# Kernel tuning notes

Measured on AMD Instinct MI355X. Metric: run time of the kernel, lower is better.

Reference implementation:

```python
import jax, jax.numpy as jnp
import numpy as np

B_, L, DM = 2, 1024, 1024
D_STATE, D_CONV, EXPAND = 16, 4, 2
DI = EXPAND * DM          # 2048 inner dim
DTR = DM // 16            # 64 dt rank


def setup_inputs() -> dict:
    key = jax.random.key(0)
    ks = jax.random.split(key, 16)
    g = lambda k, shp, s: jax.random.normal(k, shp, jnp.float32) * s
    inp = {
        "x": g(ks[0], (B_, L, DM), 1.0),
        "ln_g": jnp.ones((DM,), jnp.float32),
        "ln_b": jnp.zeros((DM,), jnp.float32),
        "in_proj_w": g(ks[1], (2 * DI, DM), (2.0 / (DM + 2 * DI)) ** 0.5),
        "conv_w": g(ks[2], (DI, 1, D_CONV), (2.0 / D_CONV) ** 0.5),
        "conv_b": jnp.zeros((DI,), jnp.float32),
        "dtin_w": g(ks[3], (DTR, DI), (2.0 / (DI + DTR)) ** 0.5),
        "dtin_b": jnp.zeros((DTR,), jnp.float32),
        "dt_w": g(ks[4], (DI, DTR), DTR ** -0.5),
        "dt_b": jnp.log(jnp.expm1(jax.random.uniform(ks[5], (DI,), jnp.float32, 1e-3, 0.1))),  # inverse-softplus of dt in [dt_min, dt_max]
        "B_w": g(ks[6], (D_STATE, DI), DI ** -0.5),
        "C_w": g(ks[7], (D_STATE, DI), DI ** -0.5),
        "A_log": jnp.log(jnp.broadcast_to(jnp.arange(1, D_STATE + 1, dtype=jnp.float32), (DI, D_STATE))),
        "D": jnp.ones((DI,), jnp.float32),
        "out_w": g(ks[8], (DM, DI), (2.0 / (DM + DI)) ** 0.5),
    }
    return inp


def _layernorm(x, g, b, eps=1e-5):
    mu = jnp.mean(x, -1, keepdims=True)
    var = jnp.mean(jnp.square(x - mu), -1, keepdims=True)
    return (x - mu) * jax.lax.rsqrt(var + eps) * g + b


def _selective_scan(u, dt, Bm, Cm, A, Dp):
    # u,dt: (b,l,di); Bm,Cm: (b,l,n); A: (di,n)
    def step(h, inp):
        dt_t, B_t, C_t, u_t = inp  # (b,di),(b,n),(b,n),(b,di)
        dA = jnp.exp(dt_t[..., None] * A)                       # (b,di,n)
        h = h * dA + (dt_t * u_t)[..., None] * B_t[:, None, :]   # (b,di,n)
        y = jnp.einsum("bdn,bn->bd", h, C_t)
        return h, y

    tm = lambda a: jnp.swapaxes(a, 0, 1)  # time-major
    h0 = jnp.zeros((u.shape[0], u.shape[2], A.shape[1]), u.dtype)
    _, ys = jax.lax.scan(step, h0, (tm(dt), tm(Bm), tm(Cm), tm(u)))
    return jnp.swapaxes(ys, 0, 1) + u * Dp  # (b,l,di)


def reference(x, ln_g, ln_b, in_proj_w, conv_w, conv_b, dtin_w, dtin_b,
              dt_w, dt_b, B_w, C_w, A_log, D, out_w):
    residual = x
    xn = _layernorm(x, ln_g, ln_b)
    xz = xn @ in_proj_w.T                       # (b,l,2*di)
    x_proj, z = jnp.split(xz, 2, axis=-1)
    # causal depthwise conv1d (left pad d_conv-1, truncate to seq_len)
    xp = jnp.pad(x_proj, ((0, 0), (D_CONV - 1, 0), (0, 0)))
    x_conv = conv_b
    for k in range(D_CONV):
        x_conv = x_conv + conv_w[:, 0, k] * xp[:, k:k + L, :]
    x_conv = jax.nn.silu(x_conv)
    dt_in = x_conv @ dtin_w.T + dtin_b          # (b,l,dtr)
    dt = jax.nn.softplus(dt_in @ dt_w.T + dt_b) # (b,l,di)
    Bm = x_conv @ B_w.T                         # (b,l,n)
    Cm = x_conv @ C_w.T
    A = -jnp.exp(A_log)                         # (di,n)
    y = _selective_scan(x_conv, dt, Bm, Cm, A, D)
    y = y * jax.nn.silu(z)
    return y @ out_w.T + residual
```

## Files before the change

kernel.cpp:

```cpp
#include <hip/hip_runtime.h>
#include <hip/hip_bf16.h>
#include <cstdint>

#define BL    2
#define LSEQ  1024
#define DMOD  1024
#define DIN   2048
#define NST   16
#define DTRK  64
#define MR    (BL*LSEQ)

#define CCH 32
#define TCH 32

typedef __bf16 bf16x8 __attribute__((ext_vector_type(8)));
typedef float  f32x4  __attribute__((ext_vector_type(4)));

#if __has_builtin(__builtin_amdgcn_exp2f)
#define EXP2F(x) __builtin_amdgcn_exp2f(x)
#else
#define EXP2F(x) exp2f(x)
#endif
#define LOG2E 1.4426950408889634f

__device__ __forceinline__ void glds16(const void* g, const void* l) {
    __builtin_amdgcn_global_load_lds(
        (__attribute__((address_space(1))) void*)(uintptr_t)(g),
        (__attribute__((address_space(3))) void*)(uint32_t)(uintptr_t)(l),
        16, 0, 0);
}

__device__ __forceinline__ __bf16 f2b(float f) {
    __hip_bfloat16 t = __float2bfloat16(f);
    return *(__bf16*)&t;
}

template <int MODE, int TM, int TN, int BK>
__global__ __launch_bounds__(256, 3) void gemm_bt(
    const __hip_bfloat16* __restrict__ A, int lda,
    const __hip_bfloat16* __restrict__ Bw, int ldb,
    int M, int N, int Ksl,
    void* __restrict__ e0, void* __restrict__ e1,
    const float* __restrict__ bias, const float* __restrict__ bias2,
    float* __restrict__ Af)
{
    constexpr bool FUSE = (MODE == 0);
    static_assert(!FUSE || BK == 64, "fused conv epilogue assumes BK=64");
    static_assert(MODE != 2 || BK == 64, "MODE 2 staging assumes BK=64");
    static_assert((MODE != 0 && MODE != 2) || TN == 128, "LDS flush assumes TN=128");
    constexpr int WM = TM / 2, WN = TN / 2;
    constexpr int MT = WM / 16, NT = WN / 16;
    constexpr int C8 = BK / 8;
    constexpr int RPP = 256 / C8;
    constexpr int PA = TM / RPP, PB = TN / RPP;
    __shared__ __align__(16) __hip_bfloat16 sA[2][TM * BK];
    __shared__ __align__(16) __hip_bfloat16 sB[2][TN * BK];
    __shared__ __align__(16) __hip_bfloat16 sH[2][(FUSE ? 16 : 1) * 64];

    auto SW = [](int row) { return (BK == 32) ? ((row >> 1) & 3) : (row & 7); };

    int bx = blockIdx.x, by = blockIdx.y;
    if ((gridDim.y & 7) == 0) {
        const int bid = blockIdx.x + gridDim.x * blockIdx.y;
        const int xcd = bid & 7, s = bid >> 3;
        const int ypx = gridDim.y >> 3;
        const int gx  = ((gridDim.x & 7) == 0) ? 8 : 1;
        const int gsz = gx * ypx;
        const int grp = s / gsz, r = s % gsz;
        bx = grp * gx + (r % gx);
        by = (r / gx) * 8 + xcd;
    }
    const int m0 = by * TM;
    const int n0 = bx * TN;
    const int k0 = blockIdx.z * Ksl;
    const int tid = threadIdx.x;
    const int w = tid >> 6, lane = tid & 63;
    const int wm = (w >> 1) * WM, wn = (w & 1) * WN;
    const int lrow = lane & 15, lq = lane >> 4;

    const int r0 = tid / C8;
    const int q = ((tid % C8) - SW(r0)) & (C8 - 1);
    const __hip_bfloat16* pa[PA];
    const __hip_bfloat16* pb[PB];
    if constexpr (MODE != 2) {
#pragma unroll
        for (int p = 0; p < PA; p++) pa[p] = A + (size_t)(m0 + r0 + RPP * p) * lda + k0 + q * 8;
    }
#pragma unroll
    for (int p = 0; p < PB; p++) pb[p] = Bw + (size_t)(n0 + r0 + RPP * p) * ldb + k0 + q * 8;

    auto stageA2 = [&](int buf, int kb) {
        if constexpr (MODE == 2) {
#pragma unroll
            for (int p = 0; p < PA; p++) {
                const int rr = r0 + RPP * p;
                const float* src = Af + (size_t)(m0 + rr) * 64 + kb * BK + q * 8;
                const float4 f0 = *(const float4*)src;
                const float4 f1 = *(const float4*)(src + 4);
                const float4 b0 = *(const float4*)&bias2[q * 8];
                const float4 b1 = *(const float4*)&bias2[q * 8 + 4];
                bf16x8 o;
                o[0] = f2b(f0.x + b0.x); o[1] = f2b(f0.y + b0.y);
                o[2] = f2b(f0.z + b0.z); o[3] = f2b(f0.w + b0.w);
                o[4] = f2b(f1.x + b1.x); o[5] = f2b(f1.y + b1.y);
                o[6] = f2b(f1.z + b1.z); o[7] = f2b(f1.w + b1.w);
                *(bf16x8*)&sA[buf][(tid + 256 * p) * 8] = o;
            }
        }
    };

    const bool isX = FUSE && (n0 < DIN);
    const __hip_bfloat16* ph = nullptr;
    if (FUSE) {
        const int rh = tid >> 3;
        const int qh = ((tid & 7) - (rh & 7)) & 7;
        ph = A + (size_t)(m0 - 16 + rh) * lda + k0 + qh * 8;
    }

    f32x4 acc[MT][NT];
#pragma unroll
    for (int i = 0; i < MT; i++)
#pragma unroll
        for (int j = 0; j < NT; j++) { acc[i][j][0]=0.f; acc[i][j][1]=0.f; acc[i][j][2]=0.f; acc[i][j][3]=0.f; }
    f32x4 hacc[FUSE ? NT : 1];
    if (FUSE)
#pragma unroll
        for (int j = 0; j < NT; j++) { hacc[j][0]=0.f; hacc[j][1]=0.f; hacc[j][2]=0.f; hacc[j][3]=0.f; }

    const int nk = Ksl / BK;
    if constexpr (MODE == 2) stageA2(0, 0);
    else {
#pragma unroll
        for (int p = 0; p < PA; p++) glds16(pa[p], &sA[0][(tid + 256 * p) * 8]);
    }
#pragma unroll
    for (int p = 0; p < PB; p++) glds16(pb[p], &sB[0][(tid + 256 * p) * 8]);
    if (isX && tid < 128) glds16(ph, &sH[0][tid * 8]);

    for (int kb = 0; kb < nk; ++kb) {
        const int cur = kb & 1, nxt = cur ^ 1;
        __syncthreads();
        if (kb + 1 < nk) {
            if constexpr (MODE == 2) stageA2(nxt, kb + 1);
            else {
#pragma unroll
                for (int p = 0; p < PA; p++) { pa[p] += BK; glds16(pa[p], &sA[nxt][(tid + 256 * p) * 8]); }
            }
#pragma unroll
            for (int p = 0; p < PB; p++) { pb[p] += BK; glds16(pb[p], &sB[nxt][(tid + 256 * p) * 8]); }
            if (isX && tid < 128) { ph += BK; glds16(ph, &sH[nxt][tid * 8]); }
        }
#pragma unroll
        for (int s = 0; s < BK / 32; s++) {
            bf16x8 af[MT], bb[NT];
#pragma unroll
            for (int mt = 0; mt < MT; mt++) {
                const int row = wm + mt * 16 + lrow;
                const int pc = ((s * 4 + lq) + SW(row)) & (C8 - 1);
                af[mt] = *(const bf16x8*)&sA[cur][row * BK + pc * 8];
            }
#pragma unroll
            for (int nt = 0; nt < NT; nt++) {
                const int row = wn + nt * 16 + lrow;
                const int pc = ((s * 4 + lq) + SW(row)) & (C8 - 1);
                bb[nt] = *(const bf16x8*)&sB[cur][row * BK + pc * 8];
            }
#pragma unroll
            for (int mt = 0; mt < MT; mt++)
#pragma unroll
                for (int nt = 0; nt < NT; nt++)
                    acc[mt][nt] = __builtin_amdgcn_mfma_f32_16x16x32_bf16(af[mt], bb[nt], acc[mt][nt], 0, 0, 0);
            if (isX && w < 2) {
                const int pcH = ((s * 4 + lq) + (lrow & 7)) & 7;
                const bf16x8 afh = *(const bf16x8*)&sH[cur][lrow * 64 + pcH * 8];
#pragma unroll
                for (int nt = 0; nt < NT; nt++)
                    hacc[nt] = __builtin_amdgcn_mfma_f32_16x16x32_bf16(afh, bb[nt], hacc[nt], 0, 0, 0);
            }
        }
    }

    if constexpr (MODE == 0) {
        if (isX) {
            __syncthreads();
            __hip_bfloat16* tile = (__hip_bfloat16*)&sB[0][0];
            constexpr int TS = TN + 8;
#pragma unroll
            for (int mt = 0; mt < MT; mt++)
#pragma unroll
                for (int nt = 0; nt < NT; nt++) {
                    const int col = wn + nt * 16 + lrow;
#pragma unroll
                    for (int r = 0; r < 4; r++)
                        tile[(16 + wm + mt * 16 + lq * 4 + r) * TS + col] = __float2bfloat16(acc[mt][nt][r]);
                }
            if (w < 2) {
#pragma unroll
                for (int nt = 0; nt < NT; nt++) {
                    const int col = wn + nt * 16 + lrow;
#pragma unroll
                    for (int r = 0; r < 4; r++)
                        tile[(lq * 4 + r) * TS + col] = __float2bfloat16(hacc[nt][r]);
                }
            }
            __syncthreads();
            const int c2 = (tid & 63) * 2;
            const int rg = tid >> 6;
            const int dg = n0 + c2;
            const float4 wA = *(const float4*)&bias[dg * 4];
            const float4 wB = *(const float4*)&bias[dg * 4 + 4];
            const float cbA = bias2[dg], cbB = bias2[dg + 1];
            const int l0 = m0 & (LSEQ - 1);
            const int rbase = rg * 16;
            float a0, a1, a2, b0, b1, b2;
            if (l0 == 0 && rg == 0) {
                a0 = a1 = a2 = b0 = b1 = b2 = 0.f;
            } else {
                const int hr = 16 + rbase - 3;
                a0 = __bfloat162float(tile[(hr + 0) * TS + c2]);
                b0 = __bfloat162float(tile[(hr + 0) * TS + c2 + 1]);
                a1 = __bfloat162float(tile[(hr + 1) * TS + c2]);
                b1 = __bfloat162float(tile[(hr + 1) * TS + c2 + 1]);
                a2 = __bfloat162float(tile[(hr + 2) * TS + c2]);
                b2 = __bfloat162float(tile[(hr + 2) * TS + c2 + 1]);
            }
            __syncthreads();
            __hip_bfloat16* xcbp = (__hip_bfloat16*)e0;
#pragma unroll 4
            for (int i = 0; i < 16; i++) {
                const int row = rbase + i;
                const float a3 = __bfloat162float(tile[(16 + row) * TS + c2]);
                const float b3 = __bfloat162float(tile[(16 + row) * TS + c2 + 1]);
                float sa = cbA + wA.x * a0 + wA.y * a1 + wA.z * a2 + wA.w * a3;
                float sb = cbB + wB.x * b0 + wB.y * b1 + wB.z * b2 + wB.w * b3;
                sa = sa / (1.f + __expf(-sa));
                sb = sb / (1.f + __expf(-sb));
                __hip_bfloat16 ha = __float2bfloat16(sa), hb = __float2bfloat16(sb);
                ushort2 o;
                o.x = (unsigned short)__hip_bfloat16_raw(ha).x;
                o.y = (unsigned short)__hip_bfloat16_raw(hb).x;
                *(ushort2*)&xcbp[(size_t)(m0 + row) * DIN + dg] = o;
                *(ushort2*)&tile[(16 + row) * TS + c2] = o;
                a0 = a1; a1 = a2; a2 = a3;
                b0 = b1; b1 = b2; b2 = b3;
            }
            __syncthreads();
            {
                const __hip_bfloat16* wpb2 = Bw + (size_t)4096 * 1024;
                const int wm2 = (w >> 1) * 32, wn2 = (w & 1) * 48;
                f32x4 acc2[2][3];
#pragma unroll
                for (int mt2 = 0; mt2 < 2; mt2++)
#pragma unroll
                    for (int nt2 = 0; nt2 < 3; nt2++) {
                        acc2[mt2][nt2][0]=0.f; acc2[mt2][nt2][1]=0.f;
                        acc2[mt2][nt2][2]=0.f; acc2[mt2][nt2][3]=0.f;
                    }
#pragma unroll
                for (int ks = 0; ks < 4; ks++) {
                    bf16x8 af2[2], bb2[3];
#pragma unroll
                    for (int mt2 = 0; mt2 < 2; mt2++)
                        af2[mt2] = *(const bf16x8*)&tile[(16 + wm2 + mt2 * 16 + lrow) * TS + ks * 32 + lq * 8];
#pragma unroll
                    for (int nt2 = 0; nt2 < 3; nt2++)
                        bb2[nt2] = *(const bf16x8*)&wpb2[(size_t)(wn2 + nt2 * 16 + lrow) * 2048 + n0 + ks * 32 + lq * 8];
#pragma unroll
                    for (int mt2 = 0; mt2 < 2; mt2++)
#pragma unroll
                        for (int nt2 = 0; nt2 < 3; nt2++)
                            acc2[mt2][nt2] = __builtin_amdgcn_mfma_f32_16x16x32_bf16(af2[mt2], bb2[nt2], acc2[mt2][nt2], 0, 0, 0);
                }
#pragma unroll
                for (int mt2 = 0; mt2 < 2; mt2++)
#pragma unroll
                    for (int nt2 = 0; nt2 < 3; nt2++) {
                        const int gn = wn2 + nt2 * 16 + lrow;
                        const int gmb = m0 + wm2 + mt2 * 16 + lq * 4;
#pragma unroll
                        for (int r = 0; r < 4; r++) {
                            const int gm = gmb + r;
                            const float v = acc2[mt2][nt2][r];
                            if (gn < 64)      atomicAdd(Af + (size_t)gm * 64 + gn, v);
                            else if (gn < 80) atomicAdd(Af + 131072 + (size_t)gm * NST + (gn - 64), v);
                            else              atomicAdd(Af + 163840 + (size_t)gm * NST + (gn - 80), v);
                        }
                    }
            }
        } else {
            __syncthreads();
            __hip_bfloat16* tile = (__hip_bfloat16*)&sB[0][0];
            constexpr int TS = TN + 8;
#pragma unroll
            for (int mt = 0; mt < MT; mt++)
#pragma unroll
                for (int nt = 0; nt < NT; nt++) {
                    const int col = wn + nt * 16 + lrow;
#pragma unroll
                    for (int r = 0; r < 4; r++) {
                        const float v = acc[mt][nt][r];
                        const float sv = v / (1.f + __expf(-v));
                        tile[(wm + mt * 16 + lq * 4 + r) * TS + col] = __float2bfloat16(sv);
                    }
                }
            __syncthreads();
            const int rr = tid >> 4, cq = (tid & 15) * 8;
            __hip_bfloat16* gz = (__hip_bfloat16*)e1 + (size_t)m0 * DIN + (n0 - DIN);
#pragma unroll
            for (int p = 0; p < TM / 16; p++)
                *(bf16x8*)(gz + (size_t)(rr + 16 * p) * DIN + cq) =
                    *(const bf16x8*)&tile[(rr + 16 * p) * TS + cq];
        }
        return;
    }
    if constexpr (MODE == 2) {
        __syncthreads();
        __hip_bfloat16* tile = (__hip_bfloat16*)&sB[0][0];
        constexpr int TS = TN + 8;
#pragma unroll
        for (int mt = 0; mt < MT; mt++)
#pragma unroll
            for (int nt = 0; nt < NT; nt++) {
                const int col = wn + nt * 16 + lrow;
                const float bv = bias[n0 + col];
#pragma unroll
                for (int r = 0; r < 4; r++) {
                    const float xx = acc[mt][nt][r] + bv;
                    const float sp = (xx > 20.f) ? xx : log1pf(__expf(xx));
                    tile[(wm + mt * 16 + lq * 4 + r) * TS + col] = __float2bfloat16(sp);
                }
            }
        __syncthreads();
        const int rr = tid >> 4, cq = (tid & 15) * 8;
        __hip_bfloat16* gy = (__hip_bfloat16*)e0 + (size_t)m0 * N + n0;
#pragma unroll
        for (int p = 0; p < TM / 16; p++)
            *(bf16x8*)(gy + (size_t)(rr + 16 * p) * N + cq) =
                *(const bf16x8*)&tile[(rr + 16 * p) * TS + cq];
        return;
    }
#pragma unroll
    for (int mt = 0; mt < MT; mt++) {
#pragma unroll
        for (int nt = 0; nt < NT; nt++) {
            const int gn = n0 + wn + nt * 16 + lrow;
            if (gn >= N) continue;
            const int gmb = m0 + wm + mt * 16 + lq * 4;
#pragma unroll
            for (int r = 0; r < 4; r++) {
                const int gm = gmb + r;
                const float v = acc[mt][nt][r];
                if (MODE == 1) {
                    if (gn < 64)      atomicAdd((float*)e0 + (size_t)gm * 64 + gn, v);
                    else if (gn < 80) atomicAdd((float*)e1 + (size_t)gm * NST + (gn - 64), v);
                    else              atomicAdd((float*)e1 + (size_t)MR * NST + (size_t)gm * NST + (gn - 80), v);
                } else {
                    ((float*)e0)[(size_t)gm * N + gn] = v + ((const float*)e1)[(size_t)gm * N + gn];
                }
            }
        }
    }
}

#define NCVT 1654784
#define NZR  49152
__global__ void prep_kernel(const float* __restrict__ x, const float* __restrict__ ln_g,
                            const float* __restrict__ ln_b,
                            const float* __restrict__ w_in, const float* __restrict__ dtin_w,
                            const float* __restrict__ B_w, const float* __restrict__ C_w,
                            const float* __restrict__ dt_w, const float* __restrict__ out_w,
                            __hip_bfloat16* __restrict__ w1b, __hip_bfloat16* __restrict__ wpb,
                            __hip_bfloat16* __restrict__ dtwb, __hip_bfloat16* __restrict__ owb,
                            __hip_bfloat16* __restrict__ xn, float* __restrict__ zblock)
{
    const int b = blockIdx.x;
    const int tid = threadIdx.x;
    if (b < MR) {
        const float4 v = ((const float4*)(x + (size_t)b * DMOD))[tid];
        float s  = v.x + v.y + v.z + v.w;
        float sq = v.x * v.x + v.y * v.y + v.z * v.z + v.w * v.w;
#pragma unroll
        for (int off = 32; off >= 1; off >>= 1) {
            s  += __shfl_down(s, off, 64);
            sq += __shfl_down(sq, off, 64);
        }
        __shared__ float red[8];
        const int w = tid >> 6, lane = tid & 63;
        if (lane == 0) { red[w] = s; red[4 + w] = sq; }
        __syncthreads();
        s  = red[0] + red[1] + red[2] + red[3];
        sq = red[4] + red[5] + red[6] + red[7];
        const float mean = s * (1.f / DMOD);
        const float rstd = rsqrtf(sq * (1.f / DMOD) - mean * mean + 1e-5f);
        const int col = tid * 4;
        const float vv[4] = {v.x, v.y, v.z, v.w};
#pragma unroll
        for (int i = 0; i < 4; i++)
            xn[(size_t)b * DMOD + col + i] =
                __float2bfloat16((vv[i] - mean) * rstd * ln_g[col + i] + ln_b[col + i]);
        return;
    }
    const int nb = gridDim.x - MR;
    for (int v4 = (b - MR) * 256 + tid; v4 < NCVT + NZR; v4 += nb * 256) {
        if (v4 >= NCVT) {
            float4 z; z.x = z.y = z.z = z.w = 0.f;
            ((float4*)zblock)[v4 - NCVT] = z;
            continue;
        }
        const int i = v4 * 4;
        const float* s; __hip_bfloat16* dk;
        if      (i < 4194304) { s = w_in   + i;             dk = w1b  + i; }
        else if (i < 4325376) { s = dtin_w + (i - 4194304); dk = wpb  + (i - 4194304); }
        else if (i < 4358144) { s = B_w    + (i - 4325376); dk = wpb  + 131072 + (i - 4325376); }
        else if (i < 4390912) { s = C_w    + (i - 4358144); dk = wpb  + 163840 + (i - 4358144); }
        else if (i < 4521984) { s = dt_w   + (i - 4390912); dk = dtwb + (i - 4390912); }
        else                  { s = out_w  + (i - 4521984); dk = owb  + (i - 4521984); }
        const float4 f = *(const float4*)s;
        ushort4 o;
        o.x = (unsigned short)(__hip_bfloat16_raw(__float2bfloat16(f.x)).x);
        o.y = (unsigned short)(__hip_bfloat16_raw(__float2bfloat16(f.y)).x);
        o.z = (unsigned short)(__hip_bfloat16_raw(__float2bfloat16(f.z)).x);
        o.w = (unsigned short)(__hip_bfloat16_raw(__float2bfloat16(f.w)).x);
        *(ushort4*)dk = o;
    }
}


__global__ __launch_bounds__(256) void scan_p1(
    const __hip_bfloat16* __restrict__ dt, const __hip_bfloat16* __restrict__ u,
    const float* __restrict__ Bm, const float* __restrict__ A_log,
    float* __restrict__ Aprod, float* __restrict__ Bacc)
{
    __shared__ float sB[TCH * NST];
    __shared__ __align__(16) __hip_bfloat16 sDT[TCH * 128];
    __shared__ __align__(16) __hip_bfloat16 sU [TCH * 128];
    const int blk = blockIdx.x;
    const int bb = blk / (CCH * 16), c = (blk >> 4) & (CCH - 1), dtile = blk & 15;
    const int tid = threadIdx.x;
    const int nh = tid & 1, dl = tid >> 1;
    const int d = dtile * 128 + dl;
    const int d0 = dtile * 128;
    const int row0 = bb * LSEQ + c * TCH;

    {
        const int r = tid >> 4, cq = (tid & 15) * 8;
        const __hip_bfloat16* gdt = dt + (size_t)row0 * DIN + d0;
        const __hip_bfloat16* gu  = u  + (size_t)row0 * DIN + d0;
#pragma unroll
        for (int p = 0; p < TCH / 16; p++) {
            glds16(gdt + (size_t)(r + 16 * p) * DIN + cq, &sDT[(r + 16 * p) * 128 + cq]);
            glds16(gu  + (size_t)(r + 16 * p) * DIN + cq, &sU [(r + 16 * p) * 128 + cq]);
        }
    }
#pragma unroll
    for (int k = 0; k < (TCH * NST) / 256; k++)
        sB[tid + 256 * k] = Bm[(size_t)row0 * NST + tid + 256 * k];

    float a2[8];
    {
        const float4 al0 = *(const float4*)&A_log[(size_t)d * NST + nh * 8];
        const float4 al1 = *(const float4*)&A_log[(size_t)d * NST + nh * 8 + 4];
        a2[0] = -__expf(al0.x) * LOG2E; a2[1] = -__expf(al0.y) * LOG2E;
        a2[2] = -__expf(al0.z) * LOG2E; a2[3] = -__expf(al0.w) * LOG2E;
        a2[4] = -__expf(al1.x) * LOG2E; a2[5] = -__expf(al1.y) * LOG2E;
        a2[6] = -__expf(al1.z) * LOG2E; a2[7] = -__expf(al1.w) * LOG2E;
    }
    __syncthreads();

    float h[8], Ap[8];
#pragma unroll
    for (int j = 0; j < 8; j++) { h[j] = 0.f; Ap[j] = 1.f; }

#pragma unroll 4
    for (int t = 0; t < TCH; t++) {
        const float dtv = __bfloat162float(sDT[t * 128 + dl]);
        const float uv  = __bfloat162float(sU [t * 128 + dl]);
        const float du = dtv * uv;
        float bv[8];
        *(float4*)&bv[0] = *(const float4*)&sB[t * NST + nh * 8];
        *(float4*)&bv[4] = *(const float4*)&sB[t * NST + nh * 8 + 4];
#pragma unroll
        for (int j = 0; j < 8; j++) {
            const float e = EXP2F(dtv * a2[j]);
            Ap[j] *= e;
            h[j] = h[j] * e + du * bv[j];
        }
    }
    const size_t idx = (((size_t)bb * CCH + c) * DIN + d) * NST + nh * 8;
    *(float4*)&Aprod[idx]     = make_float4(Ap[0], Ap[1], Ap[2], Ap[3]);
    *(float4*)&Aprod[idx + 4] = make_float4(Ap[4], Ap[5], Ap[6], Ap[7]);
    *(float4*)&Bacc[idx]      = make_float4(h[0], h[1], h[2], h[3]);
    *(float4*)&Bacc[idx + 4]  = make_float4(h[4], h[5], h[6], h[7]);
}

__global__ __launch_bounds__(256) void scan_p2(
    const float* __restrict__ Aprod, const float* __restrict__ Bacc,
    float* __restrict__ hstart)
{
    const int i = blockIdx.x * 256 + threadIdx.x;
    const int bb = i >> 15;
    const int dn = i & 32767;
    const size_t base = (((size_t)bb * CCH) << 15) + dn;
    float ap[CCH], bc[CCH];
#pragma unroll
    for (int c = 0; c < CCH; c++) {
        ap[c] = Aprod[base + ((size_t)c << 15)];
        bc[c] = Bacc[base + ((size_t)c << 15)];
    }
    float hs = 0.f;
#pragma unroll
    for (int c = 0; c < CCH; c++) {
        hstart[base + ((size_t)c << 15)] = hs;
        hs = fmaf(ap[c], hs, bc[c]);
    }
}

__global__ __launch_bounds__(256) void scan_p3(
    const __hip_bfloat16* __restrict__ dt, const __hip_bfloat16* __restrict__ u,
    const float* __restrict__ Bm, const float* __restrict__ Cm,
    const float* __restrict__ A_log, const float* __restrict__ Dp,
    const __hip_bfloat16* __restrict__ zs, const float* __restrict__ hstart,
    __hip_bfloat16* __restrict__ y)
{
    __shared__ float sB[TCH * NST], sC[TCH * NST];
    __shared__ __align__(16) __hip_bfloat16 sDT[TCH * 128];
    __shared__ __align__(16) __hip_bfloat16 sU [TCH * 128];
    __shared__ __align__(16) __hip_bfloat16 sZ [TCH * 128];
    __shared__ __align__(16) __hip_bfloat16 sY [TCH * 128];
    const int blk = blockIdx.x;
    const int bb = blk / (CCH * 16), c = (blk >> 4) & (CCH - 1), dtile = blk & 15;
    const int tid = threadIdx.x;
    const int nh = tid & 1, dl = tid >> 1;
    const int d = dtile * 128 + dl;
    const int d0 = dtile * 128;
    const int row0 = bb * LSEQ + c * TCH;

    {
        const int r = tid >> 4, cq = (tid & 15) * 8;
        const __hip_bfloat16* gdt = dt + (size_t)row0 * DIN + d0;
        const __hip_bfloat16* gu  = u  + (size_t)row0 * DIN + d0;
        const __hip_bfloat16* gz  = zs + (size_t)row0 * DIN + d0;
#pragma unroll
        for (int p = 0; p < TCH / 16; p++) {
            glds16(gdt + (size_t)(r + 16 * p) * DIN + cq, &sDT[(r + 16 * p) * 128 + cq]);
            glds16(gu  + (size_t)(r + 16 * p) * DIN + cq, &sU [(r + 16 * p) * 128 + cq]);
            glds16(gz  + (size_t)(r + 16 * p) * DIN + cq, &sZ [(r + 16 * p) * 128 + cq]);
        }
    }
#pragma unroll
    for (int k = 0; k < (TCH * NST) / 256; k++) {
        sB[tid + 256 * k] = Bm[(size_t)row0 * NST + tid + 256 * k];
        sC[tid + 256 * k] = Cm[(size_t)row0 * NST + tid + 256 * k];
    }

    float a2[8];
    {
        const float4 al0 = *(const float4*)&A_log[(size_t)d * NST + nh * 8];
        const float4 al1 = *(const float4*)&A_log[(size_t)d * NST + nh * 8 + 4];
        a2[0] = -__expf(al0.x) * LOG2E; a2[1] = -__expf(al0.y) * LOG2E;
        a2[2] = -__expf(al0.z) * LOG2E; a2[3] = -__expf(al0.w) * LOG2E;
        a2[4] = -__expf(al1.x) * LOG2E; a2[5] = -__expf(al1.y) * LOG2E;
        a2[6] = -__expf(al1.z) * LOG2E; a2[7] = -__expf(al1.w) * LOG2E;
    }
    const float Dd = Dp[d];
    const size_t idx = (((size_t)bb * CCH + c) * DIN + d) * NST + nh * 8;
    float h[8];
    *(float4*)&h[0] = *(const float4*)&hstart[idx];
    *(float4*)&h[4] = *(const float4*)&hstart[idx + 4];
    __syncthreads();

#pragma unroll 4
    for (int t = 0; t < TCH; t++) {
        const float dtv = __bfloat162float(sDT[t * 128 + dl]);
        const float uv  = __bfloat162float(sU [t * 128 + dl]);
        const float du = dtv * uv;
        float bv[8], cv[8];
        *(float4*)&bv[0] = *(const float4*)&sB[t * NST + nh * 8];
        *(float4*)&bv[4] = *(const float4*)&sB[t * NST + nh * 8 + 4];
        *(float4*)&cv[0] = *(const float4*)&sC[t * NST + nh * 8];
        *(float4*)&cv[4] = *(const float4*)&sC[t * NST + nh * 8 + 4];
        float yp = 0.f;
#pragma unroll
        for (int j = 0; j < 8; j++) {
            const float e = EXP2F(dtv * a2[j]);
            h[j] = h[j] * e + du * bv[j];
            yp += h[j] * cv[j];
        }
        yp += __shfl_xor(yp, 1, 64);
        if (nh == 0) {
            const float zv = __bfloat162float(sZ[t * 128 + dl]);
            sY[t * 128 + dl] = __float2bfloat16((yp + uv * Dd) * zv);
        }
    }
    __syncthreads();
    {
        const int r = tid >> 4, cq = (tid & 15) * 8;
        __hip_bfloat16* gy = y + (size_t)row0 * DIN + d0;
#pragma unroll
        for (int p = 0; p < TCH / 16; p++)
            *(bf16x8*)(gy + (size_t)(r + 16 * p) * DIN + cq) =
                *(const bf16x8*)&sY[(r + 16 * p) * 128 + cq];
    }
}

extern "C" void kernel_launch(void* const* d_in, const int* in_sizes, int n_in,
                              void* d_out, int out_size, void* d_ws, size_t ws_size,
                              hipStream_t stream) {
    const float* x      = (const float*)d_in[0];
    const float* ln_g   = (const float*)d_in[1];
    const float* ln_b   = (const float*)d_in[2];
    const float* w_in   = (const float*)d_in[3];
    const float* conv_w = (const float*)d_in[4];
    const float* conv_b = (const float*)d_in[5];
    const float* dtin_w = (const float*)d_in[6];
    const float* dtin_b = (const float*)d_in[7];
    const float* dt_w   = (const float*)d_in[8];
    const float* dt_b   = (const float*)d_in[9];
    const float* B_w    = (const float*)d_in[10];
    const float* C_w    = (const float*)d_in[11];
    const float* A_log  = (const float*)d_in[12];
    const float* Dp     = (const float*)d_in[13];
    const float* out_w  = (const float*)d_in[14];
    float* out = (float*)d_out;

    char* ws = (char*)d_ws;
    auto alloc = [&](size_t bytes) { char* p = ws; ws += (bytes + 255) & ~255ull; return p; };
    __hip_bfloat16* w1b   = (__hip_bfloat16*)alloc((size_t)4096 * 1024 * 2);
    __hip_bfloat16* wpb   = (__hip_bfloat16*)alloc((size_t)96 * 2048 * 2);
    __hip_bfloat16* dtwb  = (__hip_bfloat16*)alloc((size_t)2048 * 64 * 2);
    __hip_bfloat16* owb   = (__hip_bfloat16*)alloc((size_t)1024 * 2048 * 2);
    __hip_bfloat16* xnb   = (__hip_bfloat16*)alloc((size_t)MR * DMOD * 2);
    __hip_bfloat16* zs    = (__hip_bfloat16*)alloc((size_t)MR * DIN * 2);
    __hip_bfloat16* xcb   = (__hip_bfloat16*)alloc((size_t)MR * DIN * 2);
    __hip_bfloat16* dtb   = (__hip_bfloat16*)alloc((size_t)MR * DIN * 2);
    __hip_bfloat16* yb    = (__hip_bfloat16*)alloc((size_t)MR * DIN * 2);
    float*          zblock= (float*)alloc((size_t)196608 * 4);
    float*          Aprod = (float*)alloc((size_t)BL * CCH * DIN * NST * 4);
    float*          Bacc  = (float*)alloc((size_t)BL * CCH * DIN * NST * 4);
    float*          hstart= (float*)alloc((size_t)BL * CCH * DIN * NST * 4);

    float* fdtin = zblock;
    float* Bmf   = zblock + 131072;
    float* Cmf   = Bmf + (size_t)MR * NST;

    prep_kernel<<<MR + 896, 256, 0, stream>>>(x, ln_g, ln_b, w_in, dtin_w, B_w, C_w, dt_w,
                                              out_w, w1b, wpb, dtwb, owb, xnb, zblock);

    gemm_bt<0, 64, 128, 64><<<dim3(32, 32, 1), 256, 0, stream>>>(
        xnb, 1024, w1b, 1024, MR, 4096, 1024, xcb, zs, conv_w, conv_b, zblock);

    gemm_bt<2, 64, 128, 64><<<dim3(16, 32, 1), 256, 0, stream>>>(
        nullptr, 0, dtwb, 64, MR, DIN, 64, dtb, nullptr, dt_b, dtin_b, fdtin);

    scan_p1<<<BL * CCH * 16, 256, 0, stream>>>(dtb, xcb, Bmf, A_log, Aprod, Bacc);
    scan_p2<<<BL * DIN * NST / 256, 256, 0, stream>>>(Aprod, Bacc, hstart);
    scan_p3<<<BL * CCH * 16, 256, 0, stream>>>(dtb, xcb, Bmf, Cmf,
                                               A_log, Dp, zs, hstart, yb);

    gemm_bt<3, 64, 64, 64><<<dim3(16, 32, 1), 256, 0, stream>>>(
        yb, 2048, owb, 2048, MR, DMOD, 2048, out, (void*)x, nullptr, nullptr, nullptr);
}
```

Before: 219.3 us.

## Fuse dt projection GEMM and softplus into scan phase-one kernel

Removes the separate MODE-2 GEMM launch that computed dt = softplus(dt_in @ dt_w^T + b). Each scan_p1 block now computes its own 32x128 dt tile with MFMA from the fp32 dt_in rows and the bf16 dt weights, applies softplus into LDS, and writes dt out for scan_p3. This drops one kernel launch and the global re-read of dt in phase one. In exchange, scan_p1 gains MFMA work, extra registers and a longer prologue before the scan. The unused MODE 1 and MODE 2 GEMM paths are also deleted.

```diff
diff --git a/kernel.cpp b/kernel.cpp
--- a/kernel.cpp
+++ b/kernel.cpp
@@ -46,8 +46,7 @@
 {
     constexpr bool FUSE = (MODE == 0);
     static_assert(!FUSE || BK == 64, "fused conv epilogue assumes BK=64");
-    static_assert(MODE != 2 || BK == 64, "MODE 2 staging assumes BK=64");
-    static_assert((MODE != 0 && MODE != 2) || TN == 128, "LDS flush assumes TN=128");
+    static_assert((MODE != 0) || TN == 128, "LDS flush assumes TN=128");
     constexpr int WM = TM / 2, WN = TN / 2;
     constexpr int MT = WM / 16, NT = WN / 16;
     constexpr int C8 = BK / 8;
@@ -82,32 +81,10 @@
     const int q = ((tid % C8) - SW(r0)) & (C8 - 1);
     const __hip_bfloat16* pa[PA];
     const __hip_bfloat16* pb[PB];
-    if constexpr (MODE != 2) {
-#pragma unroll
-        for (int p = 0; p < PA; p++) pa[p] = A + (size_t)(m0 + r0 + RPP * p) * lda + k0 + q * 8;
-    }
+#pragma unroll
+    for (int p = 0; p < PA; p++) pa[p] = A + (size_t)(m0 + r0 + RPP * p) * lda + k0 + q * 8;
 #pragma unroll
     for (int p = 0; p < PB; p++) pb[p] = Bw + (size_t)(n0 + r0 + RPP * p) * ldb + k0 + q * 8;
-
-    auto stageA2 = [&](int buf, int kb) {
-        if constexpr (MODE == 2) {
-#pragma unroll
-            for (int p = 0; p < PA; p++) {
-                const int rr = r0 + RPP * p;
-                const float* src = Af + (size_t)(m0 + rr) * 64 + kb * BK + q * 8;
-                const float4 f0 = *(const float4*)src;
-                const float4 f1 = *(const float4*)(src + 4);
-                const float4 b0 = *(const float4*)&bias2[q * 8];
-                const float4 b1 = *(const float4*)&bias2[q * 8 + 4];
-                bf16x8 o;
-                o[0] = f2b(f0.x + b0.x); o[1] = f2b(f0.y + b0.y);
-                o[2] = f2b(f0.z + b0.z); o[3] = f2b(f0.w + b0.w);
-                o[4] = f2b(f1.x + b1.x); o[5] = f2b(f1.y + b1.y);
-                o[6] = f2b(f1.z + b1.z); o[7] = f2b(f1.w + b1.w);
-                *(bf16x8*)&sA[buf][(tid + 256 * p) * 8] = o;
-            }
-        }
-    };
 
     const bool isX = FUSE && (n0 < DIN);
     const __hip_bfloat16* ph = nullptr;
@@ -128,11 +105,8 @@
         for (int j = 0; j < NT; j++) { hacc[j][0]=0.f; hacc[j][1]=0.f; hacc[j][2]=0.f; hacc[j][3]=0.f; }
 
     const int nk = Ksl / BK;
-    if constexpr (MODE == 2) stageA2(0, 0);
-    else {
-#pragma unroll
-        for (int p = 0; p < PA; p++) glds16(pa[p], &sA[0][(tid + 256 * p) * 8]);
-    }
+#pragma unroll
+    for (int p = 0; p < PA; p++) glds16(pa[p], &sA[0][(tid + 256 * p) * 8]);
 #pragma unroll
     for (int p = 0; p < PB; p++) glds16(pb[p], &sB[0][(tid + 256 * p) * 8]);
     if (isX && tid < 128) glds16(ph, &sH[0][tid * 8]);
@@ -141,11 +115,8 @@
         const int cur = kb & 1, nxt = cur ^ 1;
         __syncthreads();
         if (kb + 1 < nk) {
-            if constexpr (MODE == 2) stageA2(nxt, kb + 1);
-            else {
-#pragma unroll
-                for (int p = 0; p < PA; p++) { pa[p] += BK; glds16(pa[p], &sA[nxt][(tid + 256 * p) * 8]); }
-            }
+#pragma unroll
+            for (int p = 0; p < PA; p++) { pa[p] += BK; glds16(pa[p], &sA[nxt][(tid + 256 * p) * 8]); }
 #pragma unroll
             for (int p = 0; p < PB; p++) { pb[p] += BK; glds16(pb[p], &sB[nxt][(tid + 256 * p) * 8]); }
             if (isX && tid < 128) { ph += BK; glds16(ph, &sH[nxt][tid * 8]); }
@@ -313,32 +284,6 @@
         }
         return;
     }
-    if constexpr (MODE == 2) {
-        __syncthreads();
-        __hip_bfloat16* tile = (__hip_bfloat16*)&sB[0][0];
-        constexpr int TS = TN + 8;
-#pragma unroll
-        for (int mt = 0; mt < MT; mt++)
-#pragma unroll
-            for (int nt = 0; nt < NT; nt++) {
-                const int col = wn + nt * 16 + lrow;
-                const float bv = bias[n0 + col];
-#pragma unroll
-                for (int r = 0; r < 4; r++) {
-                    const float xx = acc[mt][nt][r] + bv;
-                    const float sp = (xx > 20.f) ? xx : log1pf(__expf(xx));
-                    tile[(wm + mt * 16 + lq * 4 + r) * TS + col] = __float2bfloat16(sp);
-                }
-            }
-        __syncthreads();
-        const int rr = tid >> 4, cq = (tid & 15) * 8;
-        __hip_bfloat16* gy = (__hip_bfloat16*)e0 + (size_t)m0 * N + n0;
-#pragma unroll
-        for (int p = 0; p < TM / 16; p++)
-            *(bf16x8*)(gy + (size_t)(rr + 16 * p) * N + cq) =
-                *(const bf16x8*)&tile[(rr + 16 * p) * TS + cq];
-        return;
-    }
 #pragma unroll
     for (int mt = 0; mt < MT; mt++) {
 #pragma unroll
@@ -349,14 +294,7 @@
 #pragma unroll
             for (int r = 0; r < 4; r++) {
                 const int gm = gmb + r;
-                const float v = acc[mt][nt][r];
-                if (MODE == 1) {
-                    if (gn < 64)      atomicAdd((float*)e0 + (size_t)gm * 64 + gn, v);
-                    else if (gn < 80) atomicAdd((float*)e1 + (size_t)gm * NST + (gn - 64), v);
-                    else              atomicAdd((float*)e1 + (size_t)MR * NST + (size_t)gm * NST + (gn - 80), v);
-                } else {
-                    ((float*)e0)[(size_t)gm * N + gn] = v + ((const float*)e1)[(size_t)gm * N + gn];
-                }
+                ((float*)e0)[(size_t)gm * N + gn] = acc[mt][nt][r] + ((const float*)e1)[(size_t)gm * N + gn];
             }
         }
     }
@@ -427,9 +365,12 @@
 
 
 __global__ __launch_bounds__(256) void scan_p1(
-    const __hip_bfloat16* __restrict__ dt, const __hip_bfloat16* __restrict__ u,
+    const float* __restrict__ fdtin, const float* __restrict__ dtin_b,
+    const __hip_bfloat16* __restrict__ dtwb, const float* __restrict__ dt_b,
+    const __hip_bfloat16* __restrict__ u,
     const float* __restrict__ Bm, const float* __restrict__ A_log,
-    float* __restrict__ Aprod, float* __restrict__ Bacc)
+    float* __restrict__ Aprod, float* __restrict__ Bacc,
+    __hip_bfloat16* __restrict__ dtb)
 {
     __shared__ float sB[TCH * NST];
     __shared__ __align__(16) __hip_bfloat16 sDT[TCH * 128];
@@ -441,20 +382,56 @@
     const int d = dtile * 128 + dl;
     const int d0 = dtile * 128;
     const int row0 = bb * LSEQ + c * TCH;
+    const int wv = tid >> 6, lane = tid & 63;
+    const int lrow = lane & 15, lq = lane >> 4;
 
     {
         const int r = tid >> 4, cq = (tid & 15) * 8;
-        const __hip_bfloat16* gdt = dt + (size_t)row0 * DIN + d0;
-        const __hip_bfloat16* gu  = u  + (size_t)row0 * DIN + d0;
-#pragma unroll
-        for (int p = 0; p < TCH / 16; p++) {
-            glds16(gdt + (size_t)(r + 16 * p) * DIN + cq, &sDT[(r + 16 * p) * 128 + cq]);
-            glds16(gu  + (size_t)(r + 16 * p) * DIN + cq, &sU [(r + 16 * p) * 128 + cq]);
-        }
+        const __hip_bfloat16* gu = u + (size_t)row0 * DIN + d0;
+#pragma unroll
+        for (int p = 0; p < TCH / 16; p++)
+            glds16(gu + (size_t)(r + 16 * p) * DIN + cq, &sU[(r + 16 * p) * 128 + cq]);
     }
 #pragma unroll
     for (int k = 0; k < (TCH * NST) / 256; k++)
         sB[tid + 256 * k] = Bm[(size_t)row0 * NST + tid + 256 * k];
+
+    {
+        const int mt = wv >> 1;
+        const int ng = (wv & 1) * 4;
+        f32x4 dacc[4];
+#pragma unroll
+        for (int nt = 0; nt < 4; nt++) { dacc[nt][0]=0.f; dacc[nt][1]=0.f; dacc[nt][2]=0.f; dacc[nt][3]=0.f; }
+#pragma unroll
+        for (int s = 0; s < 2; s++) {
+            const float* ap = fdtin + (size_t)(row0 + mt * 16 + lrow) * 64 + s * 32 + lq * 8;
+            const float4 f0 = *(const float4*)ap;
+            const float4 f1 = *(const float4*)(ap + 4);
+            const float4 b0 = *(const float4*)&dtin_b[s * 32 + lq * 8];
+            const float4 b1 = *(const float4*)&dtin_b[s * 32 + lq * 8 + 4];
+            bf16x8 afr;
+            afr[0] = f2b(f0.x + b0.x); afr[1] = f2b(f0.y + b0.y);
+            afr[2] = f2b(f0.z + b0.z); afr[3] = f2b(f0.w + b0.w);
+            afr[4] = f2b(f1.x + b1.x); afr[5] = f2b(f1.y + b1.y);
+            afr[6] = f2b(f1.z + b1.z); afr[7] = f2b(f1.w + b1.w);
+#pragma unroll
+            for (int nt = 0; nt < 4; nt++) {
+                const bf16x8 bfr = *(const bf16x8*)&dtwb[(size_t)(d0 + (ng + nt) * 16 + lrow) * 64 + s * 32 + lq * 8];
+                dacc[nt] = __builtin_amdgcn_mfma_f32_16x16x32_bf16(afr, bfr, dacc[nt], 0, 0, 0);
+            }
+        }
+#pragma unroll
+        for (int nt = 0; nt < 4; nt++) {
+            const int dloc = (ng + nt) * 16 + lrow;
+            const float db = dt_b[d0 + dloc];
+#pragma unroll
+            for (int r = 0; r < 4; r++) {
+                const float xx = dacc[nt][r] + db;
+                const float sp = (xx > 20.f) ? xx : log1pf(__expf(xx));
+                sDT[(mt * 16 + lq * 4 + r) * 128 + dloc] = __float2bfloat16(sp);
+            }
+        }
+    }
 
     float a2[8];
     {
@@ -466,6 +443,15 @@
         a2[6] = -__expf(al1.z) * LOG2E; a2[7] = -__expf(al1.w) * LOG2E;
     }
     __syncthreads();
+
+    {
+        const int r = tid >> 4, cq = (tid & 15) * 8;
+        __hip_bfloat16* gdt = dtb + (size_t)row0 * DIN + d0;
+#pragma unroll
+        for (int p = 0; p < TCH / 16; p++)
+            *(bf16x8*)(gdt + (size_t)(r + 16 * p) * DIN + cq) =
+                *(const bf16x8*)&sDT[(r + 16 * p) * 128 + cq];
+    }
 
     float h[8], Ap[8];
 #pragma unroll
@@ -649,10 +635,8 @@
     gemm_bt<0, 64, 128, 64><<<dim3(32, 32, 1), 256, 0, stream>>>(
         xnb, 1024, w1b, 1024, MR, 4096, 1024, xcb, zs, conv_w, conv_b, zblock);
 
-    gemm_bt<2, 64, 128, 64><<<dim3(16, 32, 1), 256, 0, stream>>>(
-        nullptr, 0, dtwb, 64, MR, DIN, 64, dtb, nullptr, dt_b, dtin_b, fdtin);
-
-    scan_p1<<<BL * CCH * 16, 256, 0, stream>>>(dtb, xcb, Bmf, A_log, Aprod, Bacc);
+    scan_p1<<<BL * CCH * 16, 256, 0, stream>>>(fdtin, dtin_b, dtwb, dt_b,
+                                               xcb, Bmf, A_log, Aprod, Bacc, dtb);
     scan_p2<<<BL * DIN * NST / 256, 256, 0, stream>>>(Aprod, Bacc, hstart);
     scan_p3<<<BL * CCH * 16, 256, 0, stream>>>(dtb, xcb, Bmf, Cmf,
                                                A_log, Dp, zs, hstart, yb);
```

After: 221.6 us. About the same (+1.1%).
